# Kernel tuning notes

Hardware: AMD Instinct MI355X
Metric: run time of the kernel (lower is better)

## Reference

```python
import jax, jax.numpy as jnp
import numpy as np

H = 16  # num_heads
E = 1024  # embed_dim
HD = E // H  # head_dim = 64


def setup_inputs() -> dict:
    key = jax.random.key(0)
    k1, k2, k3 = jax.random.split(key, 3)
    n, bs = 2048, 2
    # xavier-uniform-ish scale for weights
    seq = jax.random.normal(k1, (n, bs, E), dtype=jnp.float32)
    w_qkv = jax.random.normal(k2, (3 * E, E), dtype=jnp.float32) * (2.0 / (E + 3 * E)) ** 0.5
    b_qkv = jnp.zeros((3 * E,), dtype=jnp.float32)
    w_out = jax.random.normal(k3, (E, E), dtype=jnp.float32) * (1.0 / E) ** 0.5
    b_out = jnp.zeros((E,), dtype=jnp.float32)
    return {"seq": seq, "w_qkv": w_qkv, "b_qkv": b_qkv, "w_out": w_out, "b_out": b_out}


def reference(seq, w_qkv, b_qkv, w_out, b_out):
    n, bs, _ = seq.shape
    # fused QKV projection: [n, bs, 3E]
    qkv = jnp.einsum('nbe,fe->nbf', seq, w_qkv) + b_qkv
    # reshape to [n, bs, 3, H, HD] then split -> q,k,v each [n, bs, H, HD]
    qkv = qkv.reshape(n, bs, 3, H, HD)
    q = qkv[:, :, 0] / jnp.asarray(HD, seq.dtype) ** 0.5
    k = qkv[:, :, 1]
    v = qkv[:, :, 2]
    # scores [bs, H, n, n] -- explicitly materialized as in the original
    attn = jnp.einsum('qbhd,kbhd->bhqk', q, k)
    attn = jax.nn.softmax(attn, axis=-1)
    # weighted values back to [n, bs, H, HD] -> [n, bs, E]
    out = jnp.einsum('bhqk,kbhd->qbhd', attn, v).reshape(n, bs, E)
    out = jnp.einsum('nbe,fe->nbf', out, w_out) + b_out
    return out
```

## Files before the change

kernel.cpp:

```cpp
#include <hip/hip_runtime.h>

typedef unsigned short u16;
typedef unsigned int u32;
typedef __bf16 bf16_8 __attribute__((ext_vector_type(8)));
typedef short s16x8 __attribute__((ext_vector_type(8)));
typedef short s16x4 __attribute__((ext_vector_type(4)));
typedef float f32x4 __attribute__((ext_vector_type(4)));

#define NQ 2048
#define BSZ 2
#define EDIM 1024
#define NH 16
#define HDIM 64
#define MROWS (NQ * BSZ)
#define F3 (3 * EDIM)

__device__ __forceinline__ u16 f2bf(float f) {
  u32 x = __builtin_bit_cast(u32, f);
  x += 0x7fff + ((x >> 16) & 1);
  return (u16)(x >> 16);
}
__device__ __forceinline__ void gload16(const u16* g, u16* l) {
  __builtin_amdgcn_global_load_lds(
      (const __attribute__((address_space(1))) void*)g,
      (__attribute__((address_space(3))) void*)l, 16, 0, 0);
}

__global__ __launch_bounds__(256) void cvt_f32_bf16(
    const float* __restrict__ in, u16* __restrict__ out, int n) {
  int i = (blockIdx.x * 256 + threadIdx.x) * 4;
  const int stride = gridDim.x * 256 * 4;
  for (; i < n; i += stride) {
    f32x4 v = *(const f32x4*)&in[i];
    s16x4 o;
    o[0] = (short)f2bf(v[0]);
    o[1] = (short)f2bf(v[1]);
    o[2] = (short)f2bf(v[2]);
    o[3] = (short)f2bf(v[3]);
    *(s16x4*)&out[i] = o;
  }
}

template <int MODE>
__global__ __launch_bounds__(256) void gemm_bt(
    const u16* __restrict__ A, const u16* __restrict__ B,
    const float* __restrict__ bias, int K,
    u16* __restrict__ out0, u16* __restrict__ out1, u16* __restrict__ out2,
    float* __restrict__ outf) {
  constexpr int BM = 128, BN = 128, BK = 32;
  __shared__ u16 As[BM * BK];
  __shared__ u16 Bs[BN * BK];
  const int tid = threadIdx.x;
  const int wid = tid >> 6, lane = tid & 63;
  const int wm = wid >> 1, wn = wid & 1;
  const int row0 = blockIdx.y * BM, col0 = blockIdx.x * BN;
  const int g = lane >> 4, l15 = lane & 15;
  const int lr = tid >> 2, lc8 = (tid & 3) * 8;

  f32x4 acc[4][4];
#pragma unroll
  for (int m = 0; m < 4; ++m)
#pragma unroll
    for (int n = 0; n < 4; ++n) acc[m][n] = f32x4{0.f, 0.f, 0.f, 0.f};

  for (int kb = 0; kb < K; kb += BK) {
    __syncthreads();
#pragma unroll
    for (int c = 0; c < 2; ++c) {
      gload16(&A[(size_t)(row0 + c * 64 + lr) * K + kb + lc8],
              &As[c * 2048 + wid * 512]);
      gload16(&B[(size_t)(col0 + c * 64 + lr) * K + kb + lc8],
              &Bs[c * 2048 + wid * 512]);
    }
    __syncthreads();
    bf16_8 af[4], bf[4];
#pragma unroll
    for (int m = 0; m < 4; ++m)
      af[m] = __builtin_bit_cast(
          bf16_8, *(const s16x8*)&As[(wm * 64 + m * 16 + l15) * BK + g * 8]);
#pragma unroll
    for (int n = 0; n < 4; ++n)
      bf[n] = __builtin_bit_cast(
          bf16_8, *(const s16x8*)&Bs[(wn * 64 + n * 16 + l15) * BK + g * 8]);
#pragma unroll
    for (int m = 0; m < 4; ++m)
#pragma unroll
      for (int n = 0; n < 4; ++n)
        acc[m][n] = __builtin_amdgcn_mfma_f32_16x16x32_bf16(af[m], bf[n],
                                                            acc[m][n], 0, 0, 0);
  }

  const int orow = row0 + wm * 64;
  const int ocol = col0 + wn * 64;
#pragma unroll
  for (int m = 0; m < 4; ++m) {
#pragma unroll
    for (int n = 0; n < 4; ++n) {
      const int f = ocol + n * 16 + l15;
      const float bv = bias[f];
#pragma unroll
      for (int j = 0; j < 4; ++j) {
        const int r = orow + m * 16 + g * 4 + j;
        const float v = acc[m][n][j] + bv;
        if (MODE == 0) {
          const int part = f >> 10, e = f & 1023;
          const int h = e >> 6, d = e & 63;
          const int nq = r >> 1, b = r & 1;
          const int bh = b * NH + h;
          if (part == 0)
            out0[((size_t)bh * NQ + nq) * HDIM + d] = f2bf(v * 0.125f);
          else if (part == 1)
            out1[((size_t)bh * NQ + nq) * HDIM + d] = f2bf(v);
          else
            out2[((size_t)bh * HDIM + d) * NQ + nq] = f2bf(v);
        } else {
          outf[(size_t)r * EDIM + f] = v;
        }
      }
    }
  }
}

__global__ __launch_bounds__(256) void attn_fwd(
    const u16* __restrict__ Qs, const u16* __restrict__ Ks,
    const u16* __restrict__ Vt, u16* __restrict__ AO) {
  __shared__ u16 Kt[64][72];
  __shared__ u16 Vs[64][72];
  __shared__ u16 Pl[4][2][16 * 64];
  const int tid = threadIdx.x;
  const int wid = tid >> 6, lane = tid & 63;
  const int g = lane >> 4, l15 = lane & 15;
  const int bh = blockIdx.y;
  const int qrow = blockIdx.x * 128 + wid * 32;
  const int rxor = (l15 >> 1) & 7;

  bf16_8 qf[2][2];
#pragma unroll
  for (int qb = 0; qb < 2; ++qb)
#pragma unroll
    for (int c = 0; c < 2; ++c)
      qf[qb][c] = __builtin_bit_cast(
          bf16_8, *(const s16x8*)&Qs[((size_t)bh * NQ + qrow + qb * 16 + l15) *
                                         HDIM + c * 32 + g * 8]);

  f32x4 oacc[2][4];
#pragma unroll
  for (int qb = 0; qb < 2; ++qb)
#pragma unroll
    for (int n = 0; n < 4; ++n) oacc[qb][n] = f32x4{0.f, 0.f, 0.f, 0.f};
  float rs[2][4] = {{0.f, 0.f, 0.f, 0.f}, {0.f, 0.f, 0.f, 0.f}};

  for (int kt = 0; kt < NQ; kt += 64) {
    __syncthreads();
#pragma unroll
    for (int c = 0; c < 2; ++c) {
      int id = c * 256 + tid;
      int r = id >> 3, c8 = (id & 7) * 8;
      *(s16x8*)&Kt[r][c8] =
          *(const s16x8*)&Ks[((size_t)bh * NQ + kt + r) * HDIM + c8];
      *(s16x8*)&Vs[r][c8] =
          *(const s16x8*)&Vt[((size_t)bh * HDIM + r) * NQ + kt + c8];
    }
    __syncthreads();

#pragma unroll
    for (int n = 0; n < 4; ++n) {
      bf16_8 kf0 = __builtin_bit_cast(bf16_8, *(const s16x8*)&Kt[n * 16 + l15][g * 8]);
      bf16_8 kf1 = __builtin_bit_cast(bf16_8, *(const s16x8*)&Kt[n * 16 + l15][32 + g * 8]);
      const int chunk = 2 * n + (l15 >> 3), wsub = l15 & 7;
#pragma unroll
      for (int qb = 0; qb < 2; ++qb) {
        f32x4 s = f32x4{0.f, 0.f, 0.f, 0.f};
        s = __builtin_amdgcn_mfma_f32_16x16x32_bf16(qf[qb][0], kf0, s, 0, 0, 0);
        s = __builtin_amdgcn_mfma_f32_16x16x32_bf16(qf[qb][1], kf1, s, 0, 0, 0);
#pragma unroll
        for (int j = 0; j < 4; ++j) {
          float p = __expf(s[j]);
          rs[qb][j] += p;
          const int q = g * 4 + j;
          Pl[wid][qb][q * 64 + ((chunk ^ ((q >> 1) & 7)) << 3) + wsub] = f2bf(p);
        }
      }
    }

#pragma unroll
    for (int n = 0; n < 4; ++n) {
      bf16_8 vf0 = __builtin_bit_cast(bf16_8, *(const s16x8*)&Vs[n * 16 + l15][g * 8]);
      bf16_8 vf1 = __builtin_bit_cast(bf16_8, *(const s16x8*)&Vs[n * 16 + l15][32 + g * 8]);
#pragma unroll
      for (int qb = 0; qb < 2; ++qb) {
        bf16_8 pf0 = __builtin_bit_cast(
            bf16_8, *(const s16x8*)&Pl[wid][qb][l15 * 64 + ((g ^ rxor) << 3)]);
        bf16_8 pf1 = __builtin_bit_cast(
            bf16_8, *(const s16x8*)&Pl[wid][qb][l15 * 64 + (((g + 4) ^ rxor) << 3)]);
        oacc[qb][n] = __builtin_amdgcn_mfma_f32_16x16x32_bf16(pf0, vf0, oacc[qb][n], 0, 0, 0);
        oacc[qb][n] = __builtin_amdgcn_mfma_f32_16x16x32_bf16(pf1, vf1, oacc[qb][n], 0, 0, 0);
      }
    }
  }

  const int b = bh >> 4, h = bh & 15;
#pragma unroll
  for (int qb = 0; qb < 2; ++qb) {
    float inv[4];
#pragma unroll
    for (int j = 0; j < 4; ++j) {
      float t = rs[qb][j];
      t += __shfl_xor(t, 1);
      t += __shfl_xor(t, 2);
      t += __shfl_xor(t, 4);
      t += __shfl_xor(t, 8);
      inv[j] = 1.0f / t;
    }
#pragma unroll
    for (int n = 0; n < 4; ++n)
#pragma unroll
      for (int j = 0; j < 4; ++j) {
        const int q = qrow + qb * 16 + g * 4 + j;
        AO[((size_t)q * BSZ + b) * EDIM + h * 64 + n * 16 + l15] =
            f2bf(oacc[qb][n][j] * inv[j]);
      }
  }
}

extern "C" void kernel_launch(void* const* d_in, const int* in_sizes, int n_in,
                              void* d_out, int out_size, void* d_ws,
                              size_t ws_size, hipStream_t stream) {
  const float* seq = (const float*)d_in[0];
  const float* w_qkv = (const float*)d_in[1];
  const float* b_qkv = (const float*)d_in[2];
  const float* w_out = (const float*)d_in[3];
  const float* b_out = (const float*)d_in[4];
  float* out = (float*)d_out;

  const size_t per = (size_t)BSZ * NH * NQ * HDIM;
  u16* Qs = (u16*)d_ws;
  u16* Ks = Qs + per;
  u16* Vt = Ks + per;
  u16* AO = Vt + per;
  u16* seqb = AO + (size_t)MROWS * EDIM;
  u16* wqkvb = seqb + (size_t)MROWS * EDIM;
  u16* woutb = wqkvb + (size_t)F3 * EDIM;

  cvt_f32_bf16<<<1024, 256, 0, stream>>>(seq, seqb, MROWS * EDIM);
  cvt_f32_bf16<<<1024, 256, 0, stream>>>(w_qkv, wqkvb, F3 * EDIM);
  cvt_f32_bf16<<<512, 256, 0, stream>>>(w_out, woutb, EDIM * EDIM);

  gemm_bt<0><<<dim3(F3 / 128, MROWS / 128), 256, 0, stream>>>(
      seqb, wqkvb, b_qkv, EDIM, Qs, Ks, Vt, nullptr);
  attn_fwd<<<dim3(NQ / 128, BSZ * NH), 256, 0, stream>>>(Qs, Ks, Vt, AO);
  gemm_bt<1><<<dim3(EDIM / 128, MROWS / 128), 256, 0, stream>>>(
      AO, woutb, b_out, EDIM, nullptr, nullptr, nullptr, out);
}
```

Measured before the change: 237.8 us.

## Double-buffer GEMM and attention loads, retile QKV GEMM, split attention over keys

Both GEMMs now double-buffer their shared-memory tiles using async global-to-LDS loads, so the next K-slice loads while MFMAs run. The QKV GEMM moves to 256x192 tiles with 512 threads. Attention now stages K/V through async double-buffered loads and splits the key range into two halves across grid z, doubling the block count. A new combine kernel sums the two bf16 partial outputs and divides by the summed row sums. The split adds an extra pass over memory, and storing unnormalized partials in bf16 loses some precision. Scratch buffers such as seqb and wqkvb are reused for the partials and row sums.

```diff
diff --git a/kernel.cpp b/kernel.cpp
--- a/kernel.cpp
+++ b/kernel.cpp
@@ -15,6 +15,10 @@
 #define MROWS (NQ * BSZ)
 #define F3 (3 * EDIM)
 
+__device__ __forceinline__ float bf2f(u16 u) {
+  u32 x = ((u32)u) << 16;
+  return __builtin_bit_cast(float, x);
+}
 __device__ __forceinline__ u16 f2bf(float f) {
   u32 x = __builtin_bit_cast(u32, f);
   x += 0x7fff + ((x >> 16) & 1);
@@ -41,98 +45,179 @@
   }
 }
 
-template <int MODE>
-__global__ __launch_bounds__(256) void gemm_bt(
+__global__ __launch_bounds__(512, 2) void gemm_qkv(
     const u16* __restrict__ A, const u16* __restrict__ B,
-    const float* __restrict__ bias, int K,
-    u16* __restrict__ out0, u16* __restrict__ out1, u16* __restrict__ out2,
-    float* __restrict__ outf) {
-  constexpr int BM = 128, BN = 128, BK = 32;
-  __shared__ u16 As[BM * BK];
-  __shared__ u16 Bs[BN * BK];
+    const float* __restrict__ bias,
+    u16* __restrict__ out0, u16* __restrict__ out1, u16* __restrict__ out2) {
+  constexpr int K = EDIM;
+  __shared__ u16 As[2][256 * 32];
+  __shared__ u16 Bs[2][192 * 32];
+  const int tid = threadIdx.x;
+  const int wid = tid >> 6, lane = tid & 63;
+  const int wr = wid >> 2, wc = wid & 3;
+  const int row0 = blockIdx.y * 256, col0 = blockIdx.x * 192;
+  const int g = lane >> 4, l15 = lane & 15;
+  const int lr = tid >> 2, lc8 = (tid & 3) * 8;
+
+  auto STAGE = [&](int buf, int kb) {
+    gload16(&A[(size_t)(row0 + lr) * K + kb + lc8], &As[buf][wid * 512]);
+    gload16(&A[(size_t)(row0 + 128 + lr) * K + kb + lc8],
+            &As[buf][4096 + wid * 512]);
+    gload16(&B[(size_t)(col0 + lr) * K + kb + lc8], &Bs[buf][wid * 512]);
+    if (tid < 256)
+      gload16(&B[(size_t)(col0 + 128 + lr) * K + kb + lc8],
+              &Bs[buf][4096 + wid * 512]);
+  };
+
+  f32x4 acc[8][3];
+#pragma unroll
+  for (int m = 0; m < 8; ++m)
+#pragma unroll
+    for (int n = 0; n < 3; ++n) acc[m][n] = f32x4{0.f, 0.f, 0.f, 0.f};
+
+  STAGE(0, 0);
+  __syncthreads();
+  int cur = 0;
+  for (int t = 0; t < 32; ++t) {
+    if (t < 31) STAGE(cur ^ 1, (t + 1) * 32);
+    bf16_8 af[8], bf[3];
+#pragma unroll
+    for (int m = 0; m < 8; ++m)
+      af[m] = __builtin_bit_cast(
+          bf16_8, *(const s16x8*)&As[cur][(wr * 128 + m * 16 + l15) * 32 + g * 8]);
+#pragma unroll
+    for (int n = 0; n < 3; ++n)
+      bf[n] = __builtin_bit_cast(
+          bf16_8, *(const s16x8*)&Bs[cur][(wc * 48 + n * 16 + l15) * 32 + g * 8]);
+#pragma unroll
+    for (int m = 0; m < 8; ++m)
+#pragma unroll
+      for (int n = 0; n < 3; ++n)
+        acc[m][n] = __builtin_amdgcn_mfma_f32_16x16x32_bf16(af[m], bf[n],
+                                                            acc[m][n], 0, 0, 0);
+    __syncthreads();
+    cur ^= 1;
+  }
+
+  const int orow = row0 + wr * 128;
+  const int ocol = col0 + wc * 48;
+#pragma unroll
+  for (int m = 0; m < 8; ++m) {
+#pragma unroll
+    for (int n = 0; n < 3; ++n) {
+      const int f = ocol + n * 16 + l15;
+      const float bv = bias[f];
+#pragma unroll
+      for (int j = 0; j < 4; ++j) {
+        const int r = orow + m * 16 + g * 4 + j;
+        const float v = acc[m][n][j] + bv;
+        const int part = f >> 10, e = f & 1023;
+        const int h = e >> 6, d = e & 63;
+        const int nq = r >> 1, b = r & 1;
+        const int bh = b * NH + h;
+        if (part == 0)
+          out0[((size_t)bh * NQ + nq) * HDIM + d] = f2bf(v * 0.125f);
+        else if (part == 1)
+          out1[((size_t)bh * NQ + nq) * HDIM + d] = f2bf(v);
+        else
+          out2[((size_t)bh * HDIM + d) * NQ + nq] = f2bf(v);
+      }
+    }
+  }
+}
+
+__global__ __launch_bounds__(256) void gemm_out(
+    const u16* __restrict__ A, const u16* __restrict__ B,
+    const float* __restrict__ bias, float* __restrict__ outf) {
+  constexpr int K = EDIM;
+  __shared__ u16 As[2][128 * 32];
+  __shared__ u16 Bs[2][128 * 32];
   const int tid = threadIdx.x;
   const int wid = tid >> 6, lane = tid & 63;
   const int wm = wid >> 1, wn = wid & 1;
-  const int row0 = blockIdx.y * BM, col0 = blockIdx.x * BN;
+  const int row0 = blockIdx.y * 128, col0 = blockIdx.x * 128;
   const int g = lane >> 4, l15 = lane & 15;
   const int lr = tid >> 2, lc8 = (tid & 3) * 8;
 
+  auto STAGE = [&](int buf, int kb) {
+#pragma unroll
+    for (int s = 0; s < 2; ++s) {
+      gload16(&A[(size_t)(row0 + s * 64 + lr) * K + kb + lc8],
+              &As[buf][s * 2048 + wid * 512]);
+      gload16(&B[(size_t)(col0 + s * 64 + lr) * K + kb + lc8],
+              &Bs[buf][s * 2048 + wid * 512]);
+    }
+  };
+
   f32x4 acc[4][4];
 #pragma unroll
   for (int m = 0; m < 4; ++m)
 #pragma unroll
     for (int n = 0; n < 4; ++n) acc[m][n] = f32x4{0.f, 0.f, 0.f, 0.f};
 
-  for (int kb = 0; kb < K; kb += BK) {
-    __syncthreads();
-#pragma unroll
-    for (int c = 0; c < 2; ++c) {
-      gload16(&A[(size_t)(row0 + c * 64 + lr) * K + kb + lc8],
-              &As[c * 2048 + wid * 512]);
-      gload16(&B[(size_t)(col0 + c * 64 + lr) * K + kb + lc8],
-              &Bs[c * 2048 + wid * 512]);
-    }
-    __syncthreads();
+  STAGE(0, 0);
+  __syncthreads();
+  int cur = 0;
+  for (int t = 0; t < 32; ++t) {
+    if (t < 31) STAGE(cur ^ 1, (t + 1) * 32);
     bf16_8 af[4], bf[4];
 #pragma unroll
     for (int m = 0; m < 4; ++m)
       af[m] = __builtin_bit_cast(
-          bf16_8, *(const s16x8*)&As[(wm * 64 + m * 16 + l15) * BK + g * 8]);
+          bf16_8, *(const s16x8*)&As[cur][(wm * 64 + m * 16 + l15) * 32 + g * 8]);
 #pragma unroll
     for (int n = 0; n < 4; ++n)
       bf[n] = __builtin_bit_cast(
-          bf16_8, *(const s16x8*)&Bs[(wn * 64 + n * 16 + l15) * BK + g * 8]);
+          bf16_8, *(const s16x8*)&Bs[cur][(wn * 64 + n * 16 + l15) * 32 + g * 8]);
 #pragma unroll
     for (int m = 0; m < 4; ++m)
 #pragma unroll
       for (int n = 0; n < 4; ++n)
         acc[m][n] = __builtin_amdgcn_mfma_f32_16x16x32_bf16(af[m], bf[n],
                                                             acc[m][n], 0, 0, 0);
+    __syncthreads();
+    cur ^= 1;
   }
 
   const int orow = row0 + wm * 64;
   const int ocol = col0 + wn * 64;
 #pragma unroll
-  for (int m = 0; m < 4; ++m) {
+  for (int m = 0; m < 4; ++m)
 #pragma unroll
     for (int n = 0; n < 4; ++n) {
       const int f = ocol + n * 16 + l15;
       const float bv = bias[f];
 #pragma unroll
-      for (int j = 0; j < 4; ++j) {
-        const int r = orow + m * 16 + g * 4 + j;
-        const float v = acc[m][n][j] + bv;
-        if (MODE == 0) {
-          const int part = f >> 10, e = f & 1023;
-          const int h = e >> 6, d = e & 63;
-          const int nq = r >> 1, b = r & 1;
-          const int bh = b * NH + h;
-          if (part == 0)
-            out0[((size_t)bh * NQ + nq) * HDIM + d] = f2bf(v * 0.125f);
-          else if (part == 1)
-            out1[((size_t)bh * NQ + nq) * HDIM + d] = f2bf(v);
-          else
-            out2[((size_t)bh * HDIM + d) * NQ + nq] = f2bf(v);
-        } else {
-          outf[(size_t)r * EDIM + f] = v;
-        }
-      }
-    }
-  }
-}
-
-__global__ __launch_bounds__(256) void attn_fwd(
+      for (int j = 0; j < 4; ++j)
+        outf[(size_t)(orow + m * 16 + g * 4 + j) * EDIM + f] =
+            acc[m][n][j] + bv;
+    }
+}
+
+__global__ __launch_bounds__(256) void attn_split(
     const u16* __restrict__ Qs, const u16* __restrict__ Ks,
-    const u16* __restrict__ Vt, u16* __restrict__ AO) {
-  __shared__ u16 Kt[64][72];
-  __shared__ u16 Vs[64][72];
-  __shared__ u16 Pl[4][2][16 * 64];
+    const u16* __restrict__ Vt, u16* __restrict__ op0, u16* __restrict__ op1,
+    float* __restrict__ rsp) {
+  __shared__ u16 KVs[2][8192];
+  __shared__ u16 Pl[4][2][1024];
   const int tid = threadIdx.x;
   const int wid = tid >> 6, lane = tid & 63;
   const int g = lane >> 4, l15 = lane & 15;
-  const int bh = blockIdx.y;
+  const int bh = blockIdx.y, z = blockIdx.z;
+  const int kt0 = z * (NQ / 2);
   const int qrow = blockIdx.x * 128 + wid * 32;
   const int rxor = (l15 >> 1) & 7;
+  const int r4 = tid >> 2, c8 = (tid & 3) * 8;
+
+  auto STAGE = [&](int buf, int kt) {
+#pragma unroll
+    for (int p = 0; p < 2; ++p) {
+      gload16(&Ks[((size_t)bh * NQ + kt + r4) * HDIM + p * 32 + c8],
+              &KVs[buf][p * 2048 + wid * 512]);
+      gload16(&Vt[((size_t)bh * HDIM + r4) * NQ + kt + p * 32 + c8],
+              &KVs[buf][4096 + p * 2048 + wid * 512]);
+    }
+  };
 
   bf16_8 qf[2][2];
 #pragma unroll
@@ -150,23 +235,18 @@
     for (int n = 0; n < 4; ++n) oacc[qb][n] = f32x4{0.f, 0.f, 0.f, 0.f};
   float rs[2][4] = {{0.f, 0.f, 0.f, 0.f}, {0.f, 0.f, 0.f, 0.f}};
 
-  for (int kt = 0; kt < NQ; kt += 64) {
-    __syncthreads();
-#pragma unroll
-    for (int c = 0; c < 2; ++c) {
-      int id = c * 256 + tid;
-      int r = id >> 3, c8 = (id & 7) * 8;
-      *(s16x8*)&Kt[r][c8] =
-          *(const s16x8*)&Ks[((size_t)bh * NQ + kt + r) * HDIM + c8];
-      *(s16x8*)&Vs[r][c8] =
-          *(const s16x8*)&Vt[((size_t)bh * HDIM + r) * NQ + kt + c8];
-    }
-    __syncthreads();
+  STAGE(0, kt0);
+  __syncthreads();
+  int cur = 0;
+  for (int t = 0; t < 16; ++t) {
+    if (t < 15) STAGE(cur ^ 1, kt0 + (t + 1) * 64);
 
 #pragma unroll
     for (int n = 0; n < 4; ++n) {
-      bf16_8 kf0 = __builtin_bit_cast(bf16_8, *(const s16x8*)&Kt[n * 16 + l15][g * 8]);
-      bf16_8 kf1 = __builtin_bit_cast(bf16_8, *(const s16x8*)&Kt[n * 16 + l15][32 + g * 8]);
+      bf16_8 kf0 = __builtin_bit_cast(
+          bf16_8, *(const s16x8*)&KVs[cur][(n * 16 + l15) * 32 + g * 8]);
+      bf16_8 kf1 = __builtin_bit_cast(
+          bf16_8, *(const s16x8*)&KVs[cur][2048 + (n * 16 + l15) * 32 + g * 8]);
       const int chunk = 2 * n + (l15 >> 3), wsub = l15 & 7;
 #pragma unroll
       for (int qb = 0; qb < 2; ++qb) {
@@ -185,8 +265,10 @@
 
 #pragma unroll
     for (int n = 0; n < 4; ++n) {
-      bf16_8 vf0 = __builtin_bit_cast(bf16_8, *(const s16x8*)&Vs[n * 16 + l15][g * 8]);
-      bf16_8 vf1 = __builtin_bit_cast(bf16_8, *(const s16x8*)&Vs[n * 16 + l15][32 + g * 8]);
+      bf16_8 vf0 = __builtin_bit_cast(
+          bf16_8, *(const s16x8*)&KVs[cur][4096 + (n * 16 + l15) * 32 + g * 8]);
+      bf16_8 vf1 = __builtin_bit_cast(
+          bf16_8, *(const s16x8*)&KVs[cur][6144 + (n * 16 + l15) * 32 + g * 8]);
 #pragma unroll
       for (int qb = 0; qb < 2; ++qb) {
         bf16_8 pf0 = __builtin_bit_cast(
@@ -197,30 +279,53 @@
         oacc[qb][n] = __builtin_amdgcn_mfma_f32_16x16x32_bf16(pf1, vf1, oacc[qb][n], 0, 0, 0);
       }
     }
-  }
-
+    __syncthreads();
+    cur ^= 1;
+  }
+
+  u16* op = z ? op1 : op0;
   const int b = bh >> 4, h = bh & 15;
 #pragma unroll
   for (int qb = 0; qb < 2; ++qb) {
-    float inv[4];
 #pragma unroll
     for (int j = 0; j < 4; ++j) {
-      float t = rs[qb][j];
-      t += __shfl_xor(t, 1);
-      t += __shfl_xor(t, 2);
-      t += __shfl_xor(t, 4);
-      t += __shfl_xor(t, 8);
-      inv[j] = 1.0f / t;
+      float ts = rs[qb][j];
+      ts += __shfl_xor(ts, 1);
+      ts += __shfl_xor(ts, 2);
+      ts += __shfl_xor(ts, 4);
+      ts += __shfl_xor(ts, 8);
+      if (l15 == 0)
+        rsp[(size_t)(z * 32 + bh) * NQ + qrow + qb * 16 + g * 4 + j] = ts;
     }
 #pragma unroll
     for (int n = 0; n < 4; ++n)
 #pragma unroll
       for (int j = 0; j < 4; ++j) {
         const int q = qrow + qb * 16 + g * 4 + j;
-        AO[((size_t)q * BSZ + b) * EDIM + h * 64 + n * 16 + l15] =
-            f2bf(oacc[qb][n][j] * inv[j]);
+        op[((size_t)q * BSZ + b) * EDIM + h * 64 + n * 16 + l15] =
+            f2bf(oacc[qb][n][j]);
       }
   }
+}
+
+__global__ __launch_bounds__(256) void attn_combine(
+    const u16* __restrict__ p0, const u16* __restrict__ p1,
+    const float* __restrict__ rsp, u16* __restrict__ AO) {
+  const size_t i8 = (size_t)blockIdx.x * 256 + threadIdx.x;
+  const size_t i = i8 * 8;
+  const int e = (int)(i & 1023);
+  const int b = (int)((i >> 10) & 1);
+  const int q = (int)(i >> 11);
+  const int bh = b * NH + (e >> 6);
+  const float inv = 1.0f / (rsp[(size_t)bh * NQ + q] +
+                            rsp[(size_t)(32 + bh) * NQ + q]);
+  s16x8 a = *(const s16x8*)&p0[i];
+  s16x8 c = *(const s16x8*)&p1[i];
+  s16x8 o;
+#pragma unroll
+  for (int j = 0; j < 8; ++j)
+    o[j] = (short)f2bf((bf2f((u16)a[j]) + bf2f((u16)c[j])) * inv);
+  *(s16x8*)&AO[i] = o;
 }
 
 extern "C" void kernel_launch(void* const* d_in, const int* in_sizes, int n_in,
@@ -241,14 +346,18 @@
   u16* seqb = AO + (size_t)MROWS * EDIM;
   u16* wqkvb = seqb + (size_t)MROWS * EDIM;
   u16* woutb = wqkvb + (size_t)F3 * EDIM;
+  float* rsp = (float*)wqkvb;
 
   cvt_f32_bf16<<<1024, 256, 0, stream>>>(seq, seqb, MROWS * EDIM);
   cvt_f32_bf16<<<1024, 256, 0, stream>>>(w_qkv, wqkvb, F3 * EDIM);
   cvt_f32_bf16<<<512, 256, 0, stream>>>(w_out, woutb, EDIM * EDIM);
 
-  gemm_bt<0><<<dim3(F3 / 128, MROWS / 128), 256, 0, stream>>>(
-      seqb, wqkvb, b_qkv, EDIM, Qs, Ks, Vt, nullptr);
-  attn_fwd<<<dim3(NQ / 128, BSZ * NH), 256, 0, stream>>>(Qs, Ks, Vt, AO);
-  gemm_bt<1><<<dim3(EDIM / 128, MROWS / 128), 256, 0, stream>>>(
-      AO, woutb, b_out, EDIM, nullptr, nullptr, nullptr, out);
-}
+  gemm_qkv<<<dim3(F3 / 192, MROWS / 256), 512, 0, stream>>>(
+      seqb, wqkvb, b_qkv, Qs, Ks, Vt);
+  attn_split<<<dim3(NQ / 128, BSZ * NH, 2), 256, 0, stream>>>(
+      Qs, Ks, Vt, AO, seqb, rsp);
+  attn_combine<<<(MROWS * EDIM) / (256 * 8), 256, 0, stream>>>(
+      AO, seqb, rsp, AO);
+  gemm_out<<<dim3(EDIM / 128, MROWS / 128), 256, 0, stream>>>(
+      AO, woutb, b_out, out);
+}
```

Measured after the change: 235.7 us. No clear change (-0.9%).
